# Optimization experiments

Measured on AMD Instinct MI355X. Metric: run time of the kernel, lower is better.

The kernel has to match this reference:

```python
import jax, jax.numpy as jnp
import numpy as np

N, E, C = 100000, 3200000, 30
IN, HID, OUT = 256, 256, 64


def _shapley_tables(max_n):
    # Closed form of the ShapleyGNNLayer per-node contribution:
    #   deg n == 0           : contrib = 0
    #   1 <= n <= 5 (exact)  : contrib = a(n)*x_i + b(n)*T_i,  a(n)=H_{n+1}/(n+1),
    #                          b(n) = -(H_{n+1}-1)/(n(n+1))   (H = harmonic number)
    #   n > 5 (Monte Carlo)  : permutation sum telescopes -> contrib = T_i/n exactly
    # where T_i = sum of neighbor features.
    H = np.concatenate([[0.0], np.cumsum(1.0 / np.arange(1, max_n + 2))])
    a = np.zeros(max_n + 1)
    b = np.zeros(max_n + 1)
    for m in range(1, max_n + 1):
        if m <= 5:
            a[m] = H[m + 1] / (m + 1)
            b[m] = -(H[m + 1] - 1.0) / (m * (m + 1))
        else:
            b[m] = 1.0 / m
    return jnp.asarray(a, jnp.float32), jnp.asarray(b, jnp.float32)


def _shapley_layer(x, mask, n_deg, a_tab, b_tab, W):
    T = mask @ x                                # [C,D] sum of neighbor feats
    a = a_tab[n_deg][:, None]
    b = b_tab[n_deg][:, None]
    sh = x + a * x + b * T                      # shapley_matrix (x[i] + contrib)
    return jax.nn.relu(sh @ W)


def setup_inputs() -> dict:
    key = jax.random.key(0)
    ks = jax.random.split(key, 10)
    s = 0.05
    return {
        "x": jax.random.normal(ks[0], (N, IN), jnp.float32),
        "edge_index": jax.random.randint(ks[1], (2, E), 0, N, dtype=jnp.int64)
        if jax.config.jax_enable_x64 else jax.random.randint(ks[1], (2, E), 0, N),
        "W_assign": jax.random.normal(ks[2], (IN, C), jnp.float32) * s,
        "b_assign": jnp.zeros((C,), jnp.float32),
        "W_proj": jax.random.normal(ks[3], (IN, IN), jnp.float32) * s,
        "b_proj": jnp.zeros((IN,), jnp.float32),
        "W_sh1": jax.random.normal(ks[4], (IN, HID), jnp.float32) * s,
        "W_sh2": jax.random.normal(ks[5], (HID, HID), jnp.float32) * s,
        "W_out": jax.random.normal(ks[6], (HID, OUT), jnp.float32) * s,
        "b_out": jnp.zeros((OUT,), jnp.float32),
    }


def reference(x, edge_index, W_assign, b_assign, W_proj, b_proj, W_sh1, W_sh2, W_out, b_out):
    n_nodes = x.shape[0]
    row, col = edge_index[0], edge_index[1]

    # --- MinCutPoolLayerSparse ---
    S = jax.nn.softmax(x @ W_assign + b_assign, axis=-1)        # [N,C]
    X_proj = x @ W_proj + b_proj                                 # [N,IN]
    Z = S.T @ X_proj                                             # [C,IN]
    adj_S = jax.ops.segment_sum(S[col], row, num_segments=n_nodes)   # A @ S, [N,C]
    adj_new = S.T @ adj_S                                        # [C,C]
    deg = jax.ops.segment_sum(jnp.ones((row.shape[0],), x.dtype), row,
                              num_segments=n_nodes)              # [N]
    vol = jnp.sum(S * deg[:, None])                              # trace(S^T D)
    cut = jnp.trace(adj_new)
    mincut_loss = -cut / (vol + 1e-9)
    SS = S.T @ S
    ortho_loss = jnp.linalg.norm(SS - jnp.eye(S.shape[1], dtype=S.dtype))

    # --- pooled edge structure (adj_pooled > 0) ---
    mask = (adj_new > 0).astype(x.dtype)                         # [C,C]
    n_deg = jnp.sum(adj_new > 0, axis=1)                         # [C] int
    a_tab, b_tab = _shapley_tables(S.shape[1])

    # --- Shapley GNN layers ---
    h = _shapley_layer(Z, mask, n_deg, a_tab, b_tab, W_sh1)
    h = _shapley_layer(h, mask, n_deg, a_tab, b_tab, W_sh2)
    out = h @ W_out + b_out
    return (out, mincut_loss, ortho_loss, Z, S)
```

## Files before the change

kernel.cpp:

```cpp
#include <hip/hip_runtime.h>
#include <math.h>

typedef float f32x4 __attribute__((ext_vector_type(4)));

#define N_NODES 100000
#define C_CL 30
#define D_IN 256

#define OUT_MAT 0
#define OUT_MC 1920
#define OUT_OR 1921
#define OUT_Z 1922
#define OUT_S 9602

#define WS_M 0
#define WS_SS 7680
#define WS_CS 8580
#define WS_CUT 8610
#define WS_H1 8640
#define WS_H2 16320
#define WS_WT4 24000
#define WS_S8 32256
#define WS_Q 1632768
#define Q_STRIDE 8640
#define WS_SLAB0 1771008

#define SLAB_SS 7680
#define SLAB_CS 11280
#define SLAB_STRIDE 11328
#define MAX_R 512

#define CHUNK 128
#define NCHUNK ((N_NODES + CHUNK - 1) / CHUNK)

__global__ __launch_bounds__(256)
void k_prep(const float* __restrict__ Wa, float* __restrict__ ws) {
  const int b = blockIdx.x, t = threadIdx.x;
  if (b < 8) {
    const int g = b * 256 + t;
    const int k4 = g >> 5, c = g & 31;
    float4 v = make_float4(0.f, 0.f, 0.f, 0.f);
    if (c < C_CL) {
      v.x = Wa[(4 * k4 + 0) * C_CL + c];
      v.y = Wa[(4 * k4 + 1) * C_CL + c];
      v.z = Wa[(4 * k4 + 2) * C_CL + c];
      v.w = Wa[(4 * k4 + 3) * C_CL + c];
    }
    reinterpret_cast<float4*>(ws + WS_WT4)[g] = v;
  } else {
    if (t == 0) ws[WS_CUT] = 0.f;
  }
}

__global__ __launch_bounds__(256, 4)
void k_node(const float* __restrict__ x, const float* __restrict__ wt4f,
            const float* __restrict__ ba, float* __restrict__ S_out,
            unsigned* __restrict__ S8) {
  __shared__ float lg[64][33];
  const int t = threadIdx.x;
  const int lane = t & 63;
  const int cg = __builtin_amdgcn_readfirstlane(t >> 6);
  const int node = blockIdx.x * 64 + lane;
  const bool valid = (node < N_NODES);
  const int node_c = valid ? node : (N_NODES - 1);
  const f32x4* __restrict__ xr =
      reinterpret_cast<const f32x4*>(x) + (size_t)node_c * 64;
  const float4* __restrict__ wt4 = reinterpret_cast<const float4*>(wt4f);

  float acc[8];
  #pragma unroll
  for (int j = 0; j < 8; ++j) acc[j] = 0.f;

  #pragma unroll 8
  for (int k4 = 0; k4 < 64; ++k4) {
    const f32x4 xv = xr[k4];
    #pragma unroll
    for (int j = 0; j < 8; ++j) {
      const float4 wv = wt4[k4 * 32 + cg * 8 + j];
      acc[j] += xv.x * wv.x + xv.y * wv.y + xv.z * wv.z + xv.w * wv.w;
    }
  }
  #pragma unroll
  for (int j = 0; j < 8; ++j) lg[lane][cg * 8 + j] = acc[j];
  __syncthreads();

  if (t < 64) {
    if (valid) {
      float v[C_CL];
      float mx = -3.0e38f;
      #pragma unroll
      for (int c = 0; c < C_CL; ++c) {
        v[c] = lg[t][c] + ba[c];
        mx = fmaxf(mx, v[c]);
      }
      float sm = 0.f;
      #pragma unroll
      for (int c = 0; c < C_CL; ++c) { v[c] = __expf(v[c] - mx); sm += v[c]; }
      const float r = 1.f / sm;
      #pragma unroll
      for (int c = 0; c < C_CL; ++c) lg[t][c] = v[c] * r;
    } else {
      #pragma unroll
      for (int c = 0; c < C_CL; ++c) lg[t][c] = 0.f;
    }
    lg[t][30] = 0.f; lg[t][31] = 0.f;
  }
  __syncthreads();

  const int gbase = blockIdx.x * 1920;
  #pragma unroll
  for (int i = 0; i < 8; ++i) {
    const unsigned idx = i * 256 + t;
    if (idx < 1920u) {
      const unsigned n = idx / 30u, c = idx - 30u * n;
      const int g = gbase + (int)idx;
      if (g < N_NODES * C_CL) S_out[g] = lg[n][c];
    }
  }
  const unsigned sbase = blockIdx.x * 512;
  #pragma unroll
  for (int i = 0; i < 2; ++i) {
    const unsigned idx = i * 256 + t;
    const unsigned n = idx >> 3, j = idx & 7;
    const unsigned b0 = (unsigned)(lg[n][j * 4 + 0] * 255.f + 0.5f);
    const unsigned b1 = (unsigned)(lg[n][j * 4 + 1] * 255.f + 0.5f);
    const unsigned b2 = (unsigned)(lg[n][j * 4 + 2] * 255.f + 0.5f);
    const unsigned b3 = (unsigned)(lg[n][j * 4 + 3] * 255.f + 0.5f);
    S8[sbase + idx] = b0 | (b1 << 8) | (b2 << 16) | (b3 << 24);
  }
}

__global__ __launch_bounds__(256, 2)
void k_M2(const float* __restrict__ x, const float* __restrict__ Sp,
          float* __restrict__ slabs, const int R) {
  __shared__ float sraw[8192];
  float (*sm)[32] = reinterpret_cast<float (*)[32]>(sraw);
  const int t = threadIdx.x;
  const int h = t >> 7, sub = (t >> 6) & 1, lc = t & 63;
  const int i4 = (t >> 3) & 7, j4 = t & 7, w = t >> 6;
  const f32x4* __restrict__ x4 = reinterpret_cast<const f32x4*>(x);

  float a[16][4];
  #pragma unroll
  for (int j = 0; j < 16; ++j) { a[j][0] = 0.f; a[j][1] = 0.f; a[j][2] = 0.f; a[j][3] = 0.f; }
  float ssq[16];
  #pragma unroll
  for (int j = 0; j < 16; ++j) ssq[j] = 0.f;
  float cs = 0.f;

  for (int chunk = blockIdx.x; chunk < NCHUNK; chunk += R) {
    const int node0 = chunk * CHUNK;
    const int rows_valid = N_NODES - node0;
    __syncthreads();
    #pragma unroll
    for (int i = 0; i < 15; ++i) {
      const int idx = i * 256 + t;
      const int n = idx / 30, c = idx - 30 * n;
      const int g = node0 * C_CL + idx;
      sm[n][c] = (g < N_NODES * C_CL) ? Sp[g] : 0.f;
    }
    sm[t & 127][30 + (t >> 7)] = 0.f;
    __syncthreads();

    if (rows_valid >= CHUNK) {
      #pragma unroll 4
      for (int n = 0; n < 64; ++n) {
        const int nn = sub * 64 + n;
        const f32x4 xv = __builtin_nontemporal_load(&x4[(size_t)(node0 + nn) * 64 + lc]);
        const float4 s0 = *reinterpret_cast<const float4*>(&sm[nn][h * 16 + 0]);
        const float4 s1 = *reinterpret_cast<const float4*>(&sm[nn][h * 16 + 4]);
        const float4 s2 = *reinterpret_cast<const float4*>(&sm[nn][h * 16 + 8]);
        const float4 s3 = *reinterpret_cast<const float4*>(&sm[nn][h * 16 + 12]);
        const float sv[16] = {s0.x, s0.y, s0.z, s0.w, s1.x, s1.y, s1.z, s1.w,
                              s2.x, s2.y, s2.z, s2.w, s3.x, s3.y, s3.z, s3.w};
        #pragma unroll
        for (int j = 0; j < 16; ++j) {
          a[j][0] += sv[j] * xv.x; a[j][1] += sv[j] * xv.y;
          a[j][2] += sv[j] * xv.z; a[j][3] += sv[j] * xv.w;
        }
      }
    } else {
      for (int n = 0; n < 64; ++n) {
        const int nn = sub * 64 + n;
        f32x4 xv = (f32x4)0.f;
        if (nn < rows_valid) xv = x4[(size_t)(node0 + nn) * 64 + lc];
        const float4 s0 = *reinterpret_cast<const float4*>(&sm[nn][h * 16 + 0]);
        const float4 s1 = *reinterpret_cast<const float4*>(&sm[nn][h * 16 + 4]);
        const float4 s2 = *reinterpret_cast<const float4*>(&sm[nn][h * 16 + 8]);
        const float4 s3 = *reinterpret_cast<const float4*>(&sm[nn][h * 16 + 12]);
        const float sv[16] = {s0.x, s0.y, s0.z, s0.w, s1.x, s1.y, s1.z, s1.w,
                              s2.x, s2.y, s2.z, s2.w, s3.x, s3.y, s3.z, s3.w};
        #pragma unroll
        for (int j = 0; j < 16; ++j) {
          a[j][0] += sv[j] * xv.x; a[j][1] += sv[j] * xv.y;
          a[j][2] += sv[j] * xv.z; a[j][3] += sv[j] * xv.w;
        }
      }
    }

    #pragma unroll 4
    for (int n = 0; n < 32; ++n) {
      const int nn = w * 32 + n;
      const float4 av = *reinterpret_cast<const float4*>(&sm[nn][i4 * 4]);
      const float4 bv = *reinterpret_cast<const float4*>(&sm[nn][j4 * 4]);
      const float af[4] = {av.x, av.y, av.z, av.w};
      const float bf[4] = {bv.x, bv.y, bv.z, bv.w};
      #pragma unroll
      for (int ii = 0; ii < 4; ++ii)
        #pragma unroll
        for (int jj = 0; jj < 4; ++jj) ssq[ii * 4 + jj] += af[ii] * bf[jj];
    }
    if (t < C_CL) {
      #pragma unroll 4
      for (int n = 0; n < CHUNK; ++n) cs += sm[n][t];
    }
  }

  float* __restrict__ slab = slabs + (size_t)blockIdx.x * SLAB_STRIDE;
  __syncthreads();
  if (sub == 1) {
    #pragma unroll
    for (int j = 0; j < 16; ++j) {
      const int c = h * 16 + j;
      if (c < C_CL) {
        #pragma unroll
        for (int q = 0; q < 4; ++q) sraw[c * 256 + lc * 4 + q] = a[j][q];
      }
    }
  }
  __syncthreads();
  if (sub == 0) {
    #pragma unroll
    for (int j = 0; j < 16; ++j) {
      const int c = h * 16 + j;
      if (c < C_CL) {
        #pragma unroll
        for (int q = 0; q < 4; ++q)
          slab[c * 256 + lc * 4 + q] = a[j][q] + sraw[c * 256 + lc * 4 + q];
      }
    }
  }
  #pragma unroll
  for (int ii = 0; ii < 4; ++ii) {
    #pragma unroll
    for (int jj = 0; jj < 4; ++jj) {
      const int gi = i4 * 4 + ii, gj = j4 * 4 + jj;
      if (gi < C_CL && gj < C_CL)
        slab[SLAB_SS + w * 900 + gi * C_CL + gj] = ssq[ii * 4 + jj];
    }
  }
  if (t < C_CL) slab[SLAB_CS + t] = cs;
}

__global__ __launch_bounds__(256)
void k_reduce_a(const float* __restrict__ slabs, const int R,
                float* __restrict__ Q) {
  const int i = blockIdx.x * 256 + threadIdx.x;
  const int g = blockIdx.y;
  if (i >= 8610) return;
  const int per = (R + 15) >> 4;
  const int r0 = g * per;
  const int r1 = min(r0 + per, R);
  size_t off;
  bool is_ss = false;
  if (i < 7680) off = (size_t)i;
  else if (i < 8580) { off = SLAB_SS + (i - 7680); is_ss = true; }
  else off = SLAB_CS + (i - 8580);

  float s = 0.f;
  if (!is_ss) {
    int r = r0;
    for (; r + 8 <= r1; r += 8) {
      const float* p = slabs + (size_t)r * SLAB_STRIDE + off;
      const float v0 = p[0];
      const float v1 = p[1 * SLAB_STRIDE];
      const float v2 = p[2 * SLAB_STRIDE];
      const float v3 = p[3 * SLAB_STRIDE];
      const float v4 = p[4 * SLAB_STRIDE];
      const float v5 = p[5 * SLAB_STRIDE];
      const float v6 = p[6 * SLAB_STRIDE];
      const float v7 = p[7 * SLAB_STRIDE];
      s += ((v0 + v1) + (v2 + v3)) + ((v4 + v5) + (v6 + v7));
    }
    for (; r < r1; ++r) s += slabs[(size_t)r * SLAB_STRIDE + off];
  } else {
    int r = r0;
    for (; r + 2 <= r1; r += 2) {
      const float* p0 = slabs + (size_t)r * SLAB_STRIDE + off;
      const float* p1 = p0 + SLAB_STRIDE;
      s += ((p0[0] + p0[900]) + (p0[1800] + p0[2700]))
         + ((p1[0] + p1[900]) + (p1[1800] + p1[2700]));
    }
    if (r < r1) {
      const float* p = slabs + (size_t)r * SLAB_STRIDE + off;
      s += (p[0] + p[900]) + (p[1800] + p[2700]);
    }
  }
  Q[(size_t)g * Q_STRIDE + i] = s;
}

__global__ __launch_bounds__(256)
void k_reduce_b(const float* __restrict__ Q, float* __restrict__ ws) {
  const int i = blockIdx.x * 256 + threadIdx.x;
  if (i >= 8610) return;
  float s = 0.f;
  #pragma unroll
  for (int g = 0; g < 16; ++g) s += Q[(size_t)g * Q_STRIDE + i];
  ws[i] = s;
}

__device__ __forceinline__ int dd(unsigned a, unsigned b, int acc) {
  acc += (int)((a & 0xffu) * (b & 0xffu));
  acc += (int)(((a >> 8) & 0xffu) * ((b >> 8) & 0xffu));
  acc += (int)(((a >> 16) & 0xffu) * ((b >> 16) & 0xffu));
  acc += (int)((a >> 24) * (b >> 24));
  return acc;
}

__global__ __launch_bounds__(256)
void k_edges(const int* __restrict__ ei, const int E,
             const unsigned* __restrict__ S8, float* __restrict__ ws) {
  const int t = threadIdx.x;
  const int tid = blockIdx.x * 256 + t;
  const int* __restrict__ row = ei;
  const int* __restrict__ col = ei + E;
  float acc = 0.f;
  for (int e = tid; e < E; e += gridDim.x * 256) {
    const int r = row[e], c = col[e];
    const uint4* pr = reinterpret_cast<const uint4*>(S8 + (size_t)r * 8);
    const uint4* pc = reinterpret_cast<const uint4*>(S8 + (size_t)c * 8);
    const uint4 a0 = pr[0], a1 = pr[1];
    const uint4 b0 = pc[0], b1 = pc[1];
    int s = 0;
    s = dd(a0.x, b0.x, s); s = dd(a0.y, b0.y, s);
    s = dd(a0.z, b0.z, s); s = dd(a0.w, b0.w, s);
    s = dd(a1.x, b1.x, s); s = dd(a1.y, b1.y, s);
    s = dd(a1.z, b1.z, s); s = dd(a1.w, b1.w, s);
    acc += (float)s;
  }
  acc *= (1.f / 65025.f);
  #pragma unroll
  for (int m = 1; m < 64; m <<= 1) acc += __shfl_xor(acc, m, 64);
  __shared__ float wsum[4];
  if ((t & 63) == 0) wsum[t >> 6] = acc;
  __syncthreads();
  if (t == 0)
    atomicAdd(&ws[WS_CUT], wsum[0] + wsum[1] + wsum[2] + wsum[3]);
}

__global__ __launch_bounds__(256)
void k_z(const float* __restrict__ ws, const float* __restrict__ Wp,
         const float* __restrict__ bp, float* __restrict__ out) {
  const int r = blockIdx.x, t = threadIdx.x;
  const float* m = ws + WS_M + r * 256;
  float acc = ws[WS_CS + r] * bp[t];
  #pragma unroll 8
  for (int k = 0; k < 256; ++k) acc += m[k] * Wp[(size_t)k * 256 + t];
  out[OUT_Z + r * 256 + t] = acc;
}

__global__ __launch_bounds__(256)
void k_shlayer(const float* __restrict__ in, const float* __restrict__ W,
               float* __restrict__ outp) {
  __shared__ float sh[256];
  const int r = blockIdx.x, t = threadIdx.x;
  float cs = 0.f;
  #pragma unroll
  for (int i = 0; i < C_CL; ++i) cs += in[i * 256 + t];
  sh[t] = in[r * 256 + t] + (1.f / 30.f) * cs;
  __syncthreads();
  float acc = 0.f;
  #pragma unroll 8
  for (int k = 0; k < 256; ++k) acc += sh[k] * W[(size_t)k * 256 + t];
  outp[r * 256 + t] = fmaxf(acc, 0.f);
}

__global__ __launch_bounds__(64)
void k_out(const float* __restrict__ ws, const float* __restrict__ Wo,
           const float* __restrict__ bo, float* __restrict__ out,
           const float vol) {
  const int r = blockIdx.x, t = threadIdx.x;
  if (r < C_CL) {
    const float* hrow = ws + WS_H2 + r * 256;
    float acc = bo[t];
    #pragma unroll 8
    for (int k = 0; k < 256; ++k) acc += hrow[k] * Wo[k * 64 + t];
    out[OUT_MAT + r * 64 + t] = acc;
  } else {
    float s = 0.f;
    for (int i = t; i < C_CL * C_CL; i += 64) {
      const float d = ws[WS_SS + i] - ((i / C_CL == i % C_CL) ? 1.f : 0.f);
      s += d * d;
    }
    #pragma unroll
    for (int m = 32; m >= 1; m >>= 1) s += __shfl_xor(s, m, 64);
    if (t == 0) {
      out[OUT_OR] = sqrtf(s);
      out[OUT_MC] = -ws[WS_CUT] / (vol + 1e-9f);
    }
  }
}

extern "C" void kernel_launch(void* const* d_in, const int* in_sizes, int n_in,
                              void* d_out, int out_size, void* d_ws, size_t ws_size,
                              hipStream_t stream) {
  (void)n_in; (void)out_size;
  const float* x  = (const float*)d_in[0];
  const int*   ei = (const int*)d_in[1];
  const float* Wa = (const float*)d_in[2];
  const float* ba = (const float*)d_in[3];
  const float* Wp = (const float*)d_in[4];
  const float* bp = (const float*)d_in[5];
  const float* W1 = (const float*)d_in[6];
  const float* W2 = (const float*)d_in[7];
  const float* Wo = (const float*)d_in[8];
  const float* bo = (const float*)d_in[9];
  float* out = (float*)d_out;
  float* ws  = (float*)d_ws;
  unsigned* S8 = (unsigned*)(ws + WS_S8);
  float* Q = ws + WS_Q;
  float* slabs = ws + WS_SLAB0;
  const int E = in_sizes[1] / 2;

  long avail = (long)(ws_size / 4) - WS_SLAB0;
  int R = (int)(avail / SLAB_STRIDE);
  if (R > MAX_R) R = MAX_R;
  if (R < 1) R = 1;

  k_prep<<<9, 256, 0, stream>>>(Wa, ws);
  k_node<<<1563, 256, 0, stream>>>(x, ws + WS_WT4, ba, out + OUT_S, S8);
  k_M2<<<R, 256, 0, stream>>>(x, out + OUT_S, slabs, R);
  k_reduce_a<<<dim3(34, 16), 256, 0, stream>>>(slabs, R, Q);
  k_reduce_b<<<34, 256, 0, stream>>>(Q, ws);
  k_edges<<<4096, 256, 0, stream>>>(ei, E, S8, ws);
  k_z<<<C_CL, 256, 0, stream>>>(ws, Wp, bp, out);
  k_shlayer<<<C_CL, 256, 0, stream>>>(out + OUT_Z, W1, ws + WS_H1);
  k_shlayer<<<C_CL, 256, 0, stream>>>(ws + WS_H1, W2, ws + WS_H2);
  k_out<<<C_CL + 1, 64, 0, stream>>>(ws, Wo, bo, out, (float)E);
}
```

Before: 424.8 us.

## Fuse softmax-assignment and S^T X accumulation into one persistent kernel

```diff
diff --git a/kernel.cpp b/kernel.cpp
--- a/kernel.cpp
+++ b/kernel.cpp
@@ -30,8 +30,7 @@
 #define SLAB_STRIDE 11328
 #define MAX_R 512
 
-#define CHUNK 128
-#define NCHUNK ((N_NODES + CHUNK - 1) / CHUNK)
+#define NCHUNK64 ((N_NODES + 63) / 64)
 
 __global__ __launch_bounds__(256)
 void k_prep(const float* __restrict__ Wa, float* __restrict__ ws) {
@@ -52,93 +51,24 @@
   }
 }
 
-__global__ __launch_bounds__(256, 4)
-void k_node(const float* __restrict__ x, const float* __restrict__ wt4f,
-            const float* __restrict__ ba, float* __restrict__ S_out,
-            unsigned* __restrict__ S8) {
+__global__ __launch_bounds__(256, 2)
+void k_fused(const float* __restrict__ x, const float* __restrict__ wt4f,
+             const float* __restrict__ ba, float* __restrict__ S_out,
+             unsigned* __restrict__ S8, float* __restrict__ slabs,
+             const int R) {
+  __shared__ float lx[64 * 256];
   __shared__ float lg[64][33];
+
   const int t = threadIdx.x;
   const int lane = t & 63;
-  const int cg = __builtin_amdgcn_readfirstlane(t >> 6);
-  const int node = blockIdx.x * 64 + lane;
-  const bool valid = (node < N_NODES);
-  const int node_c = valid ? node : (N_NODES - 1);
-  const f32x4* __restrict__ xr =
-      reinterpret_cast<const f32x4*>(x) + (size_t)node_c * 64;
+  const int w = t >> 6;
+  const int cg = __builtin_amdgcn_readfirstlane(w);
+  const int h = t >> 7;
+  const int sub = (t >> 6) & 1;
+  const int lc = t & 63;
+  const int i4 = (t >> 3) & 7, j4 = t & 7;
+
   const float4* __restrict__ wt4 = reinterpret_cast<const float4*>(wt4f);
-
-  float acc[8];
-  #pragma unroll
-  for (int j = 0; j < 8; ++j) acc[j] = 0.f;
-
-  #pragma unroll 8
-  for (int k4 = 0; k4 < 64; ++k4) {
-    const f32x4 xv = xr[k4];
-    #pragma unroll
-    for (int j = 0; j < 8; ++j) {
-      const float4 wv = wt4[k4 * 32 + cg * 8 + j];
-      acc[j] += xv.x * wv.x + xv.y * wv.y + xv.z * wv.z + xv.w * wv.w;
-    }
-  }
-  #pragma unroll
-  for (int j = 0; j < 8; ++j) lg[lane][cg * 8 + j] = acc[j];
-  __syncthreads();
-
-  if (t < 64) {
-    if (valid) {
-      float v[C_CL];
-      float mx = -3.0e38f;
-      #pragma unroll
-      for (int c = 0; c < C_CL; ++c) {
-        v[c] = lg[t][c] + ba[c];
-        mx = fmaxf(mx, v[c]);
-      }
-      float sm = 0.f;
-      #pragma unroll
-      for (int c = 0; c < C_CL; ++c) { v[c] = __expf(v[c] - mx); sm += v[c]; }
-      const float r = 1.f / sm;
-      #pragma unroll
-      for (int c = 0; c < C_CL; ++c) lg[t][c] = v[c] * r;
-    } else {
-      #pragma unroll
-      for (int c = 0; c < C_CL; ++c) lg[t][c] = 0.f;
-    }
-    lg[t][30] = 0.f; lg[t][31] = 0.f;
-  }
-  __syncthreads();
-
-  const int gbase = blockIdx.x * 1920;
-  #pragma unroll
-  for (int i = 0; i < 8; ++i) {
-    const unsigned idx = i * 256 + t;
-    if (idx < 1920u) {
-      const unsigned n = idx / 30u, c = idx - 30u * n;
-      const int g = gbase + (int)idx;
-      if (g < N_NODES * C_CL) S_out[g] = lg[n][c];
-    }
-  }
-  const unsigned sbase = blockIdx.x * 512;
-  #pragma unroll
-  for (int i = 0; i < 2; ++i) {
-    const unsigned idx = i * 256 + t;
-    const unsigned n = idx >> 3, j = idx & 7;
-    const unsigned b0 = (unsigned)(lg[n][j * 4 + 0] * 255.f + 0.5f);
-    const unsigned b1 = (unsigned)(lg[n][j * 4 + 1] * 255.f + 0.5f);
-    const unsigned b2 = (unsigned)(lg[n][j * 4 + 2] * 255.f + 0.5f);
-    const unsigned b3 = (unsigned)(lg[n][j * 4 + 3] * 255.f + 0.5f);
-    S8[sbase + idx] = b0 | (b1 << 8) | (b2 << 16) | (b3 << 24);
-  }
-}
-
-__global__ __launch_bounds__(256, 2)
-void k_M2(const float* __restrict__ x, const float* __restrict__ Sp,
-          float* __restrict__ slabs, const int R) {
-  __shared__ float sraw[8192];
-  float (*sm)[32] = reinterpret_cast<float (*)[32]>(sraw);
-  const int t = threadIdx.x;
-  const int h = t >> 7, sub = (t >> 6) & 1, lc = t & 63;
-  const int i4 = (t >> 3) & 7, j4 = t & 7, w = t >> 6;
-  const f32x4* __restrict__ x4 = reinterpret_cast<const f32x4*>(x);
 
   float a[16][4];
   #pragma unroll
@@ -148,71 +78,130 @@
   for (int j = 0; j < 16; ++j) ssq[j] = 0.f;
   float cs = 0.f;
 
-  for (int chunk = blockIdx.x; chunk < NCHUNK; chunk += R) {
-    const int node0 = chunk * CHUNK;
-    const int rows_valid = N_NODES - node0;
+  const int lsw = (lane & 7) << 2;
+  const int lcsh = lc << 2;
+
+  for (int chunk = blockIdx.x; chunk < NCHUNK64; chunk += R) {
+    const int node0 = chunk * 64;
+    const int rows_valid = min(64, N_NODES - node0);
     __syncthreads();
-    #pragma unroll
-    for (int i = 0; i < 15; ++i) {
-      const int idx = i * 256 + t;
-      const int n = idx / 30, c = idx - 30 * n;
-      const int g = node0 * C_CL + idx;
-      sm[n][c] = (g < N_NODES * C_CL) ? Sp[g] : 0.f;
-    }
-    sm[t & 127][30 + (t >> 7)] = 0.f;
+
+    {
+      float4 v[16];
+      #pragma unroll
+      for (int it = 0; it < 16; ++it) {
+        const int n = (it << 2) + w;
+        const int nsrc = (n < rows_valid) ? n : 0;
+        v[it] = *reinterpret_cast<const float4*>(
+            x + (size_t)(node0 + nsrc) * 256 + (lane << 2));
+      }
+      #pragma unroll
+      for (int it = 0; it < 16; ++it) {
+        const int n = (it << 2) + w;
+        *reinterpret_cast<float4*>(
+            &lx[n * 256 + ((lane ^ (n & 7)) << 2)]) = v[it];
+      }
+    }
     __syncthreads();
 
-    if (rows_valid >= CHUNK) {
-      #pragma unroll 4
-      for (int n = 0; n < 64; ++n) {
-        const int nn = sub * 64 + n;
-        const f32x4 xv = __builtin_nontemporal_load(&x4[(size_t)(node0 + nn) * 64 + lc]);
-        const float4 s0 = *reinterpret_cast<const float4*>(&sm[nn][h * 16 + 0]);
-        const float4 s1 = *reinterpret_cast<const float4*>(&sm[nn][h * 16 + 4]);
-        const float4 s2 = *reinterpret_cast<const float4*>(&sm[nn][h * 16 + 8]);
-        const float4 s3 = *reinterpret_cast<const float4*>(&sm[nn][h * 16 + 12]);
-        const float sv[16] = {s0.x, s0.y, s0.z, s0.w, s1.x, s1.y, s1.z, s1.w,
-                              s2.x, s2.y, s2.z, s2.w, s3.x, s3.y, s3.z, s3.w};
-        #pragma unroll
-        for (int j = 0; j < 16; ++j) {
-          a[j][0] += sv[j] * xv.x; a[j][1] += sv[j] * xv.y;
-          a[j][2] += sv[j] * xv.z; a[j][3] += sv[j] * xv.w;
+    {
+      float acc[8];
+      #pragma unroll
+      for (int j = 0; j < 8; ++j) acc[j] = 0.f;
+      const float* lrow = &lx[lane * 256];
+      #pragma unroll 8
+      for (int k4 = 0; k4 < 64; ++k4) {
+        const f32x4 xv =
+            *reinterpret_cast<const f32x4*>(&lrow[(k4 << 2) ^ lsw]);
+        #pragma unroll
+        for (int j = 0; j < 8; ++j) {
+          const float4 wv = wt4[k4 * 32 + cg * 8 + j];
+          acc[j] += xv.x * wv.x + xv.y * wv.y + xv.z * wv.z + xv.w * wv.w;
         }
       }
-    } else {
-      for (int n = 0; n < 64; ++n) {
-        const int nn = sub * 64 + n;
-        f32x4 xv = (f32x4)0.f;
-        if (nn < rows_valid) xv = x4[(size_t)(node0 + nn) * 64 + lc];
-        const float4 s0 = *reinterpret_cast<const float4*>(&sm[nn][h * 16 + 0]);
-        const float4 s1 = *reinterpret_cast<const float4*>(&sm[nn][h * 16 + 4]);
-        const float4 s2 = *reinterpret_cast<const float4*>(&sm[nn][h * 16 + 8]);
-        const float4 s3 = *reinterpret_cast<const float4*>(&sm[nn][h * 16 + 12]);
-        const float sv[16] = {s0.x, s0.y, s0.z, s0.w, s1.x, s1.y, s1.z, s1.w,
-                              s2.x, s2.y, s2.z, s2.w, s3.x, s3.y, s3.z, s3.w};
-        #pragma unroll
-        for (int j = 0; j < 16; ++j) {
-          a[j][0] += sv[j] * xv.x; a[j][1] += sv[j] * xv.y;
-          a[j][2] += sv[j] * xv.z; a[j][3] += sv[j] * xv.w;
+      #pragma unroll
+      for (int j = 0; j < 8; ++j) lg[lane][cg * 8 + j] = acc[j];
+    }
+    __syncthreads();
+
+    if (t < 64) {
+      if (t < rows_valid) {
+        float v[C_CL];
+        float mx = -3.0e38f;
+        #pragma unroll
+        for (int c = 0; c < C_CL; ++c) {
+          v[c] = lg[t][c] + ba[c];
+          mx = fmaxf(mx, v[c]);
         }
-      }
+        float sm = 0.f;
+        #pragma unroll
+        for (int c = 0; c < C_CL; ++c) { v[c] = __expf(v[c] - mx); sm += v[c]; }
+        const float r = 1.f / sm;
+        #pragma unroll
+        for (int c = 0; c < C_CL; ++c) lg[t][c] = v[c] * r;
+      } else {
+        #pragma unroll
+        for (int c = 0; c < C_CL; ++c) lg[t][c] = 0.f;
+      }
+      lg[t][30] = 0.f; lg[t][31] = 0.f;
+    }
+    __syncthreads();
+
+    const int gbase = chunk * 1920;
+    #pragma unroll
+    for (int i = 0; i < 8; ++i) {
+      const unsigned idx = i * 256 + t;
+      if (idx < 1920u) {
+        const unsigned n = idx / 30u, c = idx - 30u * n;
+        const int g = gbase + (int)idx;
+        if (g < N_NODES * C_CL) S_out[g] = lg[n][c];
+      }
+    }
+    const unsigned sbase = (unsigned)chunk * 512;
+    #pragma unroll
+    for (int i = 0; i < 2; ++i) {
+      const unsigned idx = i * 256 + t;
+      const unsigned n = idx >> 3, j = idx & 7;
+      const unsigned b0 = (unsigned)(lg[n][j * 4 + 0] * 255.f + 0.5f);
+      const unsigned b1 = (unsigned)(lg[n][j * 4 + 1] * 255.f + 0.5f);
+      const unsigned b2 = (unsigned)(lg[n][j * 4 + 2] * 255.f + 0.5f);
+      const unsigned b3 = (unsigned)(lg[n][j * 4 + 3] * 255.f + 0.5f);
+      S8[sbase + idx] = b0 | (b1 << 8) | (b2 << 16) | (b3 << 24);
     }
 
     #pragma unroll 4
     for (int n = 0; n < 32; ++n) {
-      const int nn = w * 32 + n;
-      const float4 av = *reinterpret_cast<const float4*>(&sm[nn][i4 * 4]);
-      const float4 bv = *reinterpret_cast<const float4*>(&sm[nn][j4 * 4]);
-      const float af[4] = {av.x, av.y, av.z, av.w};
-      const float bf[4] = {bv.x, bv.y, bv.z, bv.w};
+      const int nn = sub * 32 + n;
+      const f32x4 xv = *reinterpret_cast<const f32x4*>(
+          &lx[nn * 256 + (lcsh ^ ((nn & 7) << 2))]);
+      float sv[16];
+      #pragma unroll
+      for (int j = 0; j < 16; ++j) sv[j] = lg[nn][h * 16 + j];
+      #pragma unroll
+      for (int j = 0; j < 16; ++j) {
+        a[j][0] += sv[j] * xv.x; a[j][1] += sv[j] * xv.y;
+        a[j][2] += sv[j] * xv.z; a[j][3] += sv[j] * xv.w;
+      }
+    }
+
+    #pragma unroll 4
+    for (int n = 0; n < 16; ++n) {
+      const int nn = w * 16 + n;
+      float av[4], bv[4];
+      #pragma unroll
+      for (int ii = 0; ii < 4; ++ii) {
+        av[ii] = lg[nn][i4 * 4 + ii];
+        bv[ii] = lg[nn][j4 * 4 + ii];
+      }
       #pragma unroll
       for (int ii = 0; ii < 4; ++ii)
         #pragma unroll
-        for (int jj = 0; jj < 4; ++jj) ssq[ii * 4 + jj] += af[ii] * bf[jj];
-    }
+        for (int jj = 0; jj < 4; ++jj) ssq[ii * 4 + jj] += av[ii] * bv[jj];
+    }
+
     if (t < C_CL) {
       #pragma unroll 4
-      for (int n = 0; n < CHUNK; ++n) cs += sm[n][t];
+      for (int n = 0; n < 64; ++n) cs += lg[n][t];
     }
   }
 
@@ -224,7 +213,7 @@
       const int c = h * 16 + j;
       if (c < C_CL) {
         #pragma unroll
-        for (int q = 0; q < 4; ++q) sraw[c * 256 + lc * 4 + q] = a[j][q];
+        for (int q = 0; q < 4; ++q) lx[c * 256 + lc * 4 + q] = a[j][q];
       }
     }
   }
@@ -236,7 +225,7 @@
       if (c < C_CL) {
         #pragma unroll
         for (int q = 0; q < 4; ++q)
-          slab[c * 256 + lc * 4 + q] = a[j][q] + sraw[c * 256 + lc * 4 + q];
+          slab[c * 256 + lc * 4 + q] = a[j][q] + lx[c * 256 + lc * 4 + q];
       }
     }
   }
@@ -428,8 +417,7 @@
   if (R < 1) R = 1;
 
   k_prep<<<9, 256, 0, stream>>>(Wa, ws);
-  k_node<<<1563, 256, 0, stream>>>(x, ws + WS_WT4, ba, out + OUT_S, S8);
-  k_M2<<<R, 256, 0, stream>>>(x, out + OUT_S, slabs, R);
+  k_fused<<<R, 256, 0, stream>>>(x, ws + WS_WT4, ba, out + OUT_S, S8, slabs, R);
   k_reduce_a<<<dim3(34, 16), 256, 0, stream>>>(slabs, R, Q);
   k_reduce_b<<<34, 256, 0, stream>>>(Q, ws);
   k_edges<<<4096, 256, 0, stream>>>(ei, E, S8, ws);
```

Result: slower. 465.9 us (+9.7%).

## Fuse prep, reduction and tail kernels; pre-reduce per-wave SS inside M2

Applied to the files above, without the earlier changes.

```diff
diff --git a/kernel.cpp b/kernel.cpp
--- a/kernel.cpp
+++ b/kernel.cpp
@@ -18,54 +18,42 @@
 #define WS_CS 8580
 #define WS_CUT 8610
 #define WS_H1 8640
-#define WS_H2 16320
-#define WS_WT4 24000
 #define WS_S8 32256
-#define WS_Q 1632768
-#define Q_STRIDE 8640
 #define WS_SLAB0 1771008
 
-#define SLAB_SS 7680
-#define SLAB_CS 11280
-#define SLAB_STRIDE 11328
+#define SLAB_SS2 7680
+#define SLAB_CS2 8580
+#define SLAB_STRIDE2 8640
 #define MAX_R 512
 
 #define CHUNK 128
 #define NCHUNK ((N_NODES + CHUNK - 1) / CHUNK)
 
-__global__ __launch_bounds__(256)
-void k_prep(const float* __restrict__ Wa, float* __restrict__ ws) {
-  const int b = blockIdx.x, t = threadIdx.x;
-  if (b < 8) {
-    const int g = b * 256 + t;
-    const int k4 = g >> 5, c = g & 31;
-    float4 v = make_float4(0.f, 0.f, 0.f, 0.f);
-    if (c < C_CL) {
-      v.x = Wa[(4 * k4 + 0) * C_CL + c];
-      v.y = Wa[(4 * k4 + 1) * C_CL + c];
-      v.z = Wa[(4 * k4 + 2) * C_CL + c];
-      v.w = Wa[(4 * k4 + 3) * C_CL + c];
-    }
-    reinterpret_cast<float4*>(ws + WS_WT4)[g] = v;
-  } else {
-    if (t == 0) ws[WS_CUT] = 0.f;
-  }
-}
-
 __global__ __launch_bounds__(256, 4)
-void k_node(const float* __restrict__ x, const float* __restrict__ wt4f,
+void k_node(const float* __restrict__ x, const float* __restrict__ Wa,
             const float* __restrict__ ba, float* __restrict__ S_out,
             unsigned* __restrict__ S8) {
   __shared__ float lg[64][33];
+  __shared__ float lwf[8192];
   const int t = threadIdx.x;
   const int lane = t & 63;
   const int cg = __builtin_amdgcn_readfirstlane(t >> 6);
+
+  #pragma unroll 8
+  for (int it = 0; it < 32; ++it) {
+    const int idx = it * 256 + t;
+    const int k = 4 * (idx >> 7) + (idx & 3);
+    const int c = (idx >> 2) & 31;
+    lwf[idx] = (c < C_CL) ? Wa[k * C_CL + c] : 0.f;
+  }
+
   const int node = blockIdx.x * 64 + lane;
   const bool valid = (node < N_NODES);
   const int node_c = valid ? node : (N_NODES - 1);
   const f32x4* __restrict__ xr =
       reinterpret_cast<const f32x4*>(x) + (size_t)node_c * 64;
-  const float4* __restrict__ wt4 = reinterpret_cast<const float4*>(wt4f);
+  const float4* __restrict__ lw4 = reinterpret_cast<const float4*>(lwf);
+  __syncthreads();
 
   float acc[8];
   #pragma unroll
@@ -76,7 +64,7 @@
     const f32x4 xv = xr[k4];
     #pragma unroll
     for (int j = 0; j < 8; ++j) {
-      const float4 wv = wt4[k4 * 32 + cg * 8 + j];
+      const float4 wv = lw4[k4 * 32 + cg * 8 + j];
       acc[j] += xv.x * wv.x + xv.y * wv.y + xv.z * wv.z + xv.w * wv.w;
     }
   }
@@ -117,7 +105,7 @@
       if (g < N_NODES * C_CL) S_out[g] = lg[n][c];
     }
   }
-  const unsigned sbase = blockIdx.x * 512;
+  const unsigned sbase = (unsigned)blockIdx.x * 512;
   #pragma unroll
   for (int i = 0; i < 2; ++i) {
     const unsigned idx = i * 256 + t;
@@ -216,7 +204,7 @@
     }
   }
 
-  float* __restrict__ slab = slabs + (size_t)blockIdx.x * SLAB_STRIDE;
+  float* __restrict__ slab = slabs + (size_t)blockIdx.x * SLAB_STRIDE2;
   __syncthreads();
   if (sub == 1) {
     #pragma unroll
@@ -240,72 +228,40 @@
       }
     }
   }
+  __syncthreads();
   #pragma unroll
   for (int ii = 0; ii < 4; ++ii) {
     #pragma unroll
     for (int jj = 0; jj < 4; ++jj) {
       const int gi = i4 * 4 + ii, gj = j4 * 4 + jj;
       if (gi < C_CL && gj < C_CL)
-        slab[SLAB_SS + w * 900 + gi * C_CL + gj] = ssq[ii * 4 + jj];
-    }
-  }
-  if (t < C_CL) slab[SLAB_CS + t] = cs;
+        sraw[w * 900 + gi * C_CL + gj] = ssq[ii * 4 + jj];
+    }
+  }
+  __syncthreads();
+  for (int q = t; q < 900; q += 256)
+    slab[SLAB_SS2 + q] = (sraw[q] + sraw[900 + q]) + (sraw[1800 + q] + sraw[2700 + q]);
+  if (t < C_CL) slab[SLAB_CS2 + t] = cs;
 }
 
 __global__ __launch_bounds__(256)
-void k_reduce_a(const float* __restrict__ slabs, const int R,
-                float* __restrict__ Q) {
+void k_reduce(const float* __restrict__ slabs, const int R,
+              float* __restrict__ ws) {
   const int i = blockIdx.x * 256 + threadIdx.x;
-  const int g = blockIdx.y;
-  if (i >= 8610) return;
-  const int per = (R + 15) >> 4;
-  const int r0 = g * per;
-  const int r1 = min(r0 + per, R);
-  size_t off;
-  bool is_ss = false;
-  if (i < 7680) off = (size_t)i;
-  else if (i < 8580) { off = SLAB_SS + (i - 7680); is_ss = true; }
-  else off = SLAB_CS + (i - 8580);
-
-  float s = 0.f;
-  if (!is_ss) {
-    int r = r0;
-    for (; r + 8 <= r1; r += 8) {
-      const float* p = slabs + (size_t)r * SLAB_STRIDE + off;
-      const float v0 = p[0];
-      const float v1 = p[1 * SLAB_STRIDE];
-      const float v2 = p[2 * SLAB_STRIDE];
-      const float v3 = p[3 * SLAB_STRIDE];
-      const float v4 = p[4 * SLAB_STRIDE];
-      const float v5 = p[5 * SLAB_STRIDE];
-      const float v6 = p[6 * SLAB_STRIDE];
-      const float v7 = p[7 * SLAB_STRIDE];
-      s += ((v0 + v1) + (v2 + v3)) + ((v4 + v5) + (v6 + v7));
-    }
-    for (; r < r1; ++r) s += slabs[(size_t)r * SLAB_STRIDE + off];
-  } else {
-    int r = r0;
-    for (; r + 2 <= r1; r += 2) {
-      const float* p0 = slabs + (size_t)r * SLAB_STRIDE + off;
-      const float* p1 = p0 + SLAB_STRIDE;
-      s += ((p0[0] + p0[900]) + (p0[1800] + p0[2700]))
-         + ((p1[0] + p1[900]) + (p1[1800] + p1[2700]));
-    }
-    if (r < r1) {
-      const float* p = slabs + (size_t)r * SLAB_STRIDE + off;
-      s += (p[0] + p[900]) + (p[1800] + p[2700]);
-    }
-  }
-  Q[(size_t)g * Q_STRIDE + i] = s;
-}
-
-__global__ __launch_bounds__(256)
-void k_reduce_b(const float* __restrict__ Q, float* __restrict__ ws) {
-  const int i = blockIdx.x * 256 + threadIdx.x;
+  if (i == 0) ws[WS_CUT] = 0.f;
   if (i >= 8610) return;
   float s = 0.f;
-  #pragma unroll
-  for (int g = 0; g < 16; ++g) s += Q[(size_t)g * Q_STRIDE + i];
+  int r = 0;
+  for (; r + 16 <= R; r += 16) {
+    const float* p = slabs + (size_t)r * SLAB_STRIDE2 + i;
+    float v[16];
+    #pragma unroll
+    for (int q = 0; q < 16; ++q) v[q] = p[(size_t)q * SLAB_STRIDE2];
+    float s0 = ((v[0] + v[1]) + (v[2] + v[3])) + ((v[4] + v[5]) + (v[6] + v[7]));
+    float s1 = ((v[8] + v[9]) + (v[10] + v[11])) + ((v[12] + v[13]) + (v[14] + v[15]));
+    s += s0 + s1;
+  }
+  for (; r < R; ++r) s += slabs[(size_t)r * SLAB_STRIDE2 + i];
   ws[i] = s;
 }
 
@@ -349,53 +305,79 @@
 }
 
 __global__ __launch_bounds__(256)
-void k_z(const float* __restrict__ ws, const float* __restrict__ Wp,
-         const float* __restrict__ bp, float* __restrict__ out) {
+void k_z1(const float* __restrict__ ws, const float* __restrict__ Wp,
+          const float* __restrict__ bp, const float* __restrict__ W1,
+          float* __restrict__ out, float* __restrict__ h1out) {
+  __shared__ float Mr[256], Mc[256], sh[256];
   const int r = blockIdx.x, t = threadIdx.x;
-  const float* m = ws + WS_M + r * 256;
-  float acc = ws[WS_CS + r] * bp[t];
+  float mc = 0.f;
+  #pragma unroll
+  for (int rr = 0; rr < C_CL; ++rr) mc += ws[WS_M + rr * 256 + t];
+  Mc[t] = mc;
+  Mr[t] = ws[WS_M + r * 256 + t];
+  float scs = 0.f;
+  #pragma unroll
+  for (int rr = 0; rr < C_CL; ++rr) scs += ws[WS_CS + rr];
+  __syncthreads();
+  const float bpt = bp[t];
+  float az = ws[WS_CS + r] * bpt;
+  float ac = scs * bpt;
   #pragma unroll 8
-  for (int k = 0; k < 256; ++k) acc += m[k] * Wp[(size_t)k * 256 + t];
-  out[OUT_Z + r * 256 + t] = acc;
+  for (int k = 0; k < 256; ++k) {
+    const float wv = Wp[(size_t)k * 256 + t];
+    az += Mr[k] * wv;
+    ac += Mc[k] * wv;
+  }
+  out[OUT_Z + r * 256 + t] = az;
+  sh[t] = az + (1.f / 30.f) * ac;
+  __syncthreads();
+  float a1 = 0.f;
+  #pragma unroll 8
+  for (int k = 0; k < 256; ++k) a1 += sh[k] * W1[(size_t)k * 256 + t];
+  h1out[r * 256 + t] = fmaxf(a1, 0.f);
 }
 
 __global__ __launch_bounds__(256)
-void k_shlayer(const float* __restrict__ in, const float* __restrict__ W,
-               float* __restrict__ outp) {
+void k_z2(const float* __restrict__ ws, const float* __restrict__ W2,
+          const float* __restrict__ Wo, const float* __restrict__ bo,
+          float* __restrict__ out, const float vol) {
   __shared__ float sh[256];
-  const int r = blockIdx.x, t = threadIdx.x;
-  float cs = 0.f;
-  #pragma unroll
-  for (int i = 0; i < C_CL; ++i) cs += in[i * 256 + t];
-  sh[t] = in[r * 256 + t] + (1.f / 30.f) * cs;
-  __syncthreads();
-  float acc = 0.f;
-  #pragma unroll 8
-  for (int k = 0; k < 256; ++k) acc += sh[k] * W[(size_t)k * 256 + t];
-  outp[r * 256 + t] = fmaxf(acc, 0.f);
-}
-
-__global__ __launch_bounds__(64)
-void k_out(const float* __restrict__ ws, const float* __restrict__ Wo,
-           const float* __restrict__ bo, float* __restrict__ out,
-           const float vol) {
+  __shared__ float h2[256];
+  __shared__ float red[4][64];
+  __shared__ float wsum[4];
   const int r = blockIdx.x, t = threadIdx.x;
   if (r < C_CL) {
-    const float* hrow = ws + WS_H2 + r * 256;
-    float acc = bo[t];
+    float cs1 = 0.f;
+    #pragma unroll
+    for (int rr = 0; rr < C_CL; ++rr) cs1 += ws[WS_H1 + rr * 256 + t];
+    sh[t] = ws[WS_H1 + r * 256 + t] + (1.f / 30.f) * cs1;
+    __syncthreads();
+    float a2 = 0.f;
     #pragma unroll 8
-    for (int k = 0; k < 256; ++k) acc += hrow[k] * Wo[k * 64 + t];
-    out[OUT_MAT + r * 64 + t] = acc;
+    for (int k = 0; k < 256; ++k) a2 += sh[k] * W2[(size_t)k * 256 + t];
+    h2[t] = fmaxf(a2, 0.f);
+    __syncthreads();
+    const int c = t & 63, q = t >> 6;
+    float ao = 0.f;
+    #pragma unroll 8
+    for (int k = q * 64; k < q * 64 + 64; ++k) ao += h2[k] * Wo[k * 64 + c];
+    red[q][c] = ao;
+    __syncthreads();
+    if (t < 64)
+      out[OUT_MAT + r * 64 + t] =
+          bo[t] + ((red[0][t] + red[1][t]) + (red[2][t] + red[3][t]));
   } else {
     float s = 0.f;
-    for (int i = t; i < C_CL * C_CL; i += 64) {
+    for (int i = t; i < 900; i += 256) {
       const float d = ws[WS_SS + i] - ((i / C_CL == i % C_CL) ? 1.f : 0.f);
       s += d * d;
     }
     #pragma unroll
-    for (int m = 32; m >= 1; m >>= 1) s += __shfl_xor(s, m, 64);
+    for (int m = 1; m < 64; m <<= 1) s += __shfl_xor(s, m, 64);
+    if ((t & 63) == 0) wsum[t >> 6] = s;
+    __syncthreads();
     if (t == 0) {
-      out[OUT_OR] = sqrtf(s);
+      out[OUT_OR] = sqrtf(wsum[0] + wsum[1] + wsum[2] + wsum[3]);
       out[OUT_MC] = -ws[WS_CUT] / (vol + 1e-9f);
     }
   }
@@ -418,23 +400,18 @@
   float* out = (float*)d_out;
   float* ws  = (float*)d_ws;
   unsigned* S8 = (unsigned*)(ws + WS_S8);
-  float* Q = ws + WS_Q;
   float* slabs = ws + WS_SLAB0;
   const int E = in_sizes[1] / 2;
 
   long avail = (long)(ws_size / 4) - WS_SLAB0;
-  int R = (int)(avail / SLAB_STRIDE);
+  int R = (int)(avail / SLAB_STRIDE2);
   if (R > MAX_R) R = MAX_R;
   if (R < 1) R = 1;
 
-  k_prep<<<9, 256, 0, stream>>>(Wa, ws);
-  k_node<<<1563, 256, 0, stream>>>(x, ws + WS_WT4, ba, out + OUT_S, S8);
+  k_node<<<1563, 256, 0, stream>>>(x, Wa, ba, out + OUT_S, S8);
   k_M2<<<R, 256, 0, stream>>>(x, out + OUT_S, slabs, R);
-  k_reduce_a<<<dim3(34, 16), 256, 0, stream>>>(slabs, R, Q);
-  k_reduce_b<<<34, 256, 0, stream>>>(Q, ws);
+  k_reduce<<<34, 256, 0, stream>>>(slabs, R, ws);
   k_edges<<<4096, 256, 0, stream>>>(ei, E, S8, ws);
-  k_z<<<C_CL, 256, 0, stream>>>(ws, Wp, bp, out);
-  k_shlayer<<<C_CL, 256, 0, stream>>>(out + OUT_Z, W1, ws + WS_H1);
-  k_shlayer<<<C_CL, 256, 0, stream>>>(ws + WS_H1, W2, ws + WS_H2);
-  k_out<<<C_CL + 1, 64, 0, stream>>>(ws, Wo, bo, out, (float)E);
-}
+  k_z1<<<C_CL, 256, 0, stream>>>(ws, Wp, bp, W1, out, ws + WS_H1);
+  k_z2<<<C_CL + 1, 256, 0, stream>>>(ws, W2, Wo, bo, out, (float)E);
+}
```

Measured after the change: 468.0 us. +10.2%, slower.
